# Kernel optimization log

Measured on AMD Instinct MI355X. Metric: run time of the kernel, lower is better.

## Reference

```python
import jax, jax.numpy as jnp
import numpy as np
from jax import lax

B, C, H, W = 16, 128, 64, 64
S = 16  # d_state


def setup_inputs() -> dict:
    key = jax.random.key(0)
    ks = jax.random.split(key, 12)
    d = {
        'x': jax.random.normal(ks[0], (B, C, H, W), jnp.float32),
        'conv_w': jax.random.normal(ks[1], (C, C, 3, 3), jnp.float32) * (1.0 / np.sqrt(C * 9)),
        'conv_b': jax.random.normal(ks[2], (C,), jnp.float32) * 0.01,
        'dt_w': jax.random.normal(ks[3], (C, C), jnp.float32) * (1.0 / np.sqrt(C)),
        'dt_b': jax.random.normal(ks[4], (C,), jnp.float32) * 0.01,
        'A': jax.random.normal(ks[5], (C, S), jnp.float32),
        'D': jax.random.normal(ks[6], (C,), jnp.float32),
        'g1_w': jax.random.normal(ks[7], (C, C), jnp.float32) * (1.0 / np.sqrt(C)),
        'g1_b': jax.random.normal(ks[8], (C,), jnp.float32) * 0.01,
        'g2_w': jax.random.normal(ks[9], (C, C), jnp.float32) * (1.0 / np.sqrt(C)),
        'g2_b': jax.random.normal(ks[10], (C,), jnp.float32) * 0.01,
    }
    return d


def _forward(x, conv_w, conv_b, dt_w, dt_b, A, D, g1_w, g1_b, g2_w, g2_b):
    identity = x
    # 3x3 conv, padding=1 (SAME)
    x = lax.conv_general_dilated(x, conv_w, (1, 1), 'SAME',
                                 dimension_numbers=('NCHW', 'OIHW', 'NCHW'))
    x = x + conv_b[None, :, None, None]
    # spectral gate: global avg pool -> 1x1 conv -> relu -> 1x1 conv -> sigmoid
    pooled = jnp.mean(x, axis=(2, 3))                       # [B, C]
    g = jax.nn.relu(jnp.einsum('bc,oc->bo', pooled, g1_w) + g1_b)
    g = jax.nn.sigmoid(jnp.einsum('bc,oc->bo', g, g2_w) + g2_b)
    x = x * g[:, :, None, None]
    # ssm scan over H*W tokens
    x_seq = x.transpose(0, 2, 3, 1).reshape(x.shape[0], H * W, C)  # [B, L, C]
    dt = jax.nn.sigmoid(jnp.einsum('blc,oc->blo', x_seq, dt_w) + dt_b)
    An = -jnp.exp(A)   # [C, S]
    Dp = jnp.exp(D)    # [C]

    def step(h, inp):
        xt, dtt = inp  # each [B, C]
        h = h * jnp.exp(An[None] * dtt[:, :, None]) + xt[:, :, None]  # [B, C, S]
        y = jnp.sum(h * An[None], axis=-1) + Dp * xt                   # [B, C]
        return h, y

    h0 = jnp.zeros((x.shape[0], C, S), x.dtype)
    xs = (x_seq.transpose(1, 0, 2), dt.transpose(1, 0, 2))  # [L, B, C]
    _, ys = lax.scan(step, h0, xs)                           # ys: [L, B, C]
    y = ys.transpose(1, 0, 2).reshape(x.shape[0], H, W, C).transpose(0, 3, 1, 2)
    return y + identity


def reference(x, conv_w, conv_b, dt_w, dt_b, A, D, g1_w, g1_b, g2_w, g2_b):
    return _forward(x, conv_w, conv_b, dt_w, dt_b, A, D, g1_w, g1_b, g2_w, g2_b)
```

## Files before the change

kernel.cpp:

```cpp
#include <hip/hip_runtime.h>
#include <hip/hip_bf16.h>
#include <stdint.h>

#define BB 16
#define CC 128
#define HH 64
#define WW 64
#define LL 4096
#define SS 16
#define NCH 64
#define CT 64

typedef __attribute__((ext_vector_type(2))) float f32x2;
typedef __attribute__((ext_vector_type(4))) float f32x4;
typedef __attribute__((ext_vector_type(8))) short short8;
typedef __attribute__((ext_vector_type(4))) unsigned int u32x4;

#define AS1 __attribute__((address_space(1)))
#define AS3 __attribute__((address_space(3)))

__device__ __forceinline__ float bf2f(unsigned short u) {
    union { unsigned int i; float f; } v;
    v.i = ((unsigned int)u) << 16;
    return v.f;
}
__device__ __forceinline__ float asf(unsigned int u) {
    union { unsigned int i; float f; } v;
    v.i = u;
    return v.f;
}
__device__ __forceinline__ unsigned short f2bf(float f) {
    union { float f; unsigned int i; } v;
    v.f = f;
    unsigned int x = v.i;
    return (unsigned short)((x + 0x7fffu + ((x >> 16) & 1u)) >> 16);
}
__device__ __forceinline__ float fexp2(float x) { return __builtin_amdgcn_exp2f(x); }

__global__ __launch_bounds__(256) void k0(const float* __restrict__ x, unsigned short* __restrict__ xT,
                                          const float* __restrict__ conv_w, const float* __restrict__ dt_w,
                                          const float* __restrict__ A, const float* __restrict__ Dv,
                                          const float* __restrict__ g1w, const float* __restrict__ g2w,
                                          short* __restrict__ wf, short* __restrict__ wdtf,
                                          float* __restrict__ An, float* __restrict__ An2, float* __restrict__ Dp,
                                          float* __restrict__ pooled, float* __restrict__ g1wT, float* __restrict__ g2wT) {
    __shared__ float lt[64][65];
    int bid = blockIdx.x;
    int tid = threadIdx.x;
    if (bid < 2048) {
        int b = bid >> 7, rem = bid & 127;
        int tt = rem >> 1, ct = rem & 1;
        int t0 = tt * 64, c0 = ct * 64;
        int colr = tid & 63, rowb = tid >> 6;
#pragma unroll
        for (int r = 0; r < 16; ++r) {
            int row = rowb + r * 4;
            lt[row][colr] = x[(size_t)(b * CC + c0 + row) * LL + t0 + colr];
        }
        __syncthreads();
#pragma unroll
        for (int r = 0; r < 16; ++r) {
            int trow = rowb + r * 4;
            xT[((size_t)b * LL + t0 + trow) * CC + c0 + colr] = f2bf(lt[colr][trow]);
        }
        return;
    }
    int idx = (bid - 2048) * 256 + tid;
    if (idx < 18432) {
        int lane = idx & 63, fr = idx >> 6;
        int nfg = fr & 7, ks = (fr >> 3) & 3, tp = fr >> 5;
        int dy = tp / 3, dx = tp % 3;
        int cout = nfg * 16 + (lane & 15);
        int cin0 = ks * 32 + (lane >> 4) * 8;
        short8 v;
#pragma unroll
        for (int j = 0; j < 8; ++j)
            v[j] = (short)f2bf(conv_w[((cout * CC + cin0 + j) * 3 + dy) * 3 + dx]);
        *(short8*)(wf + (size_t)idx * 8) = v;
    } else if (idx < 20480) {
        int i2 = idx - 18432;
        int lane = i2 & 63, fr = i2 >> 6;
        int nfg = fr & 7, ks = fr >> 3;
        int o = nfg * 16 + (lane & 15);
        int c0 = ks * 32 + (lane >> 4) * 8;
        short8 v;
#pragma unroll
        for (int j = 0; j < 8; ++j) v[j] = (short)f2bf(dt_w[o * CC + c0 + j]);
        *(short8*)(wdtf + (size_t)i2 * 8) = v;
    } else if (idx < 22528) {
        int i3 = idx - 20480;
        float a = -expf(A[i3]);
        An[i3] = a;
        An2[i3] = a * 1.4426950408889634f;
    } else if (idx < 22656) {
        int c = idx - 22528;
        Dp[c] = expf(Dv[c]);
    } else if (idx < 24704) {
        pooled[idx - 22656] = 0.f;
    } else if (idx < 41088) {
        int i = idx - 24704;
        int c = i >> 7, o = i & 127;
        g1wT[i] = g1w[o * 128 + c];
    } else if (idx < 57472) {
        int i = idx - 41088;
        int c = i >> 7, o = i & 127;
        g2wT[i] = g2w[o * 128 + c];
    }
}

__global__ __launch_bounds__(256) void k1(const unsigned short* __restrict__ xT,
                                          const short* __restrict__ wf,
                                          const float* __restrict__ conv_b,
                                          unsigned short* __restrict__ convT,
                                          float* __restrict__ pooled) {
    __shared__ __align__(16) unsigned short slab[3 * 66 * 128];
    int bid = blockIdx.x;
    int b = bid >> 6, h = bid & 63;
    int tid = threadIdx.x;
    int wave = tid >> 6, lane = tid & 63;

    if (tid < 96) {
        int dy = tid >> 5, r = (tid >> 4) & 1, j = tid & 15;
        u32x4 z = {0, 0, 0, 0};
        *(u32x4*)((char*)slab + dy * 16896 + (r ? 16640 : 0) + j * 16) = z;
    }
#pragma unroll
    for (int dy = 0; dy < 3; ++dy) {
        int hs = h + dy - 1;
        char* slabdy = (char*)slab + dy * 16896;
        if (hs >= 0 && hs < HH) {
            const char* src = (const char*)xT + (size_t)(b * LL + hs * 64) * 256;
#pragma unroll
            for (int i = 0; i < 4; ++i) {
                unsigned int Xbase = 256u + (unsigned)i * 4096u + (unsigned)wave * 1024u;
                unsigned int X = Xbase + (unsigned)lane * 16u;
                unsigned int tok = X >> 8;
                unsigned int srcoff = ((X & ~255u) - 256u) | ((X & 255u) ^ ((tok & 7u) << 4));
                __builtin_amdgcn_global_load_lds((const AS1 unsigned int*)(src + srcoff),
                                                 (AS3 unsigned int*)(slabdy + Xbase), 16, 0, 0);
            }
        } else {
            u32x4 z = {0, 0, 0, 0};
#pragma unroll
            for (int i = 0; i < 4; ++i)
                *(u32x4*)(slabdy + 256 + tid * 64 + i * 16) = z;
        }
    }
    __syncthreads();

    int lm = lane & 15, lg = lane >> 4;
    f32x4 acc[4][2];
#pragma unroll
    for (int m = 0; m < 4; ++m)
#pragma unroll
        for (int n = 0; n < 2; ++n) acc[m][n] = (f32x4){0.f, 0.f, 0.f, 0.f};

#pragma unroll
    for (int tp = 0; tp < 9; ++tp) {
        int dy = tp / 3, dx = tp % 3;
        const char* slabdy = (const char*)slab + dy * 16896;
#pragma unroll
        for (int ks = 0; ks < 4; ++ks) {
            short8 bf0 = *(const short8*)(wf + ((size_t)(((tp * 4 + ks) * 8) + wave * 2 + 0) * 64 + lane) * 8);
            short8 bf1 = *(const short8*)(wf + ((size_t)(((tp * 4 + ks) * 8) + wave * 2 + 1) * 64 + lane) * 8);
#pragma unroll
            for (int mf = 0; mf < 4; ++mf) {
                int tok = mf * 16 + lm + dx;
                unsigned int off = (unsigned)((tok * 256 + ks * 64 + lg * 16) ^ ((tok & 7) << 4));
                short8 af = *(const short8*)(slabdy + off);
                acc[mf][0] = __builtin_amdgcn_mfma_f32_16x16x32_bf16(af, bf0, acc[mf][0], 0, 0, 0);
                acc[mf][1] = __builtin_amdgcn_mfma_f32_16x16x32_bf16(af, bf1, acc[mf][1], 0, 0, 0);
            }
        }
    }

    int n0w = wave * 32;
    size_t tokbase = (size_t)(b * LL + h * 64);
    float psum[2] = {0.f, 0.f};
#pragma unroll
    for (int nf = 0; nf < 2; ++nf) {
        int n = n0w + nf * 16 + lm;
        float bias = conv_b[n];
#pragma unroll
        for (int mf = 0; mf < 4; ++mf)
#pragma unroll
            for (int r = 0; r < 4; ++r) {
                int w = mf * 16 + lg * 4 + r;
                float v = acc[mf][nf][r] + bias;
                convT[(tokbase + w) * CC + n] = f2bf(v);
                psum[nf] += v;
            }
    }
#pragma unroll
    for (int nf = 0; nf < 2; ++nf) {
        float s = psum[nf];
        s += __shfl_xor(s, 16);
        s += __shfl_xor(s, 32);
        if (lane < 16) atomicAdd(&pooled[b * CC + n0w + nf * 16 + lane], s);
    }
}

__global__ __launch_bounds__(256) void k3(const unsigned short* __restrict__ convT,
                                          const short* __restrict__ wdtf,
                                          const float* __restrict__ pooled,
                                          const float* __restrict__ g1wT, const float* __restrict__ g1b,
                                          const float* __restrict__ g2wT, const float* __restrict__ g2b,
                                          float* __restrict__ gate,
                                          const float* __restrict__ dt_b,
                                          const float* __restrict__ An2,
                                          unsigned short* __restrict__ dtT,
                                          unsigned int* __restrict__ xdt,
                                          float* __restrict__ hend, float* __restrict__ decay,
                                          int packed) {
    __shared__ __align__(16) unsigned short albuf[128 * 128];
    __shared__ __align__(16) unsigned short dtl[128 * 136];
    __shared__ float gl[128];
    float* meanr = (float*)dtl;
    float* garr  = ((float*)dtl) + 128;
    int bid = blockIdx.x;
    int b = bid >> 5, tile = bid & 31, t0 = tile * 128;
    int tid = threadIdx.x;
    int wave = tid >> 6, lane = tid & 63;

    if (tid < 128) meanr[tid] = pooled[b * CC + tid] * (1.f / 4096.f);
    __syncthreads();
    if (tid < 128) {
        float acc = g1b[tid];
        for (int c = 0; c < 128; ++c) acc += meanr[c] * g1wT[c * 128 + tid];
        garr[tid] = fmaxf(acc, 0.f);
    }
    __syncthreads();
    if (tid < 128) {
        float acc2 = g2b[tid];
        for (int c = 0; c < 128; ++c) acc2 += garr[c] * g2wT[c * 128 + tid];
        float gv = __builtin_amdgcn_rcpf(1.f + fexp2(-1.4426950408889634f * acc2));
        gl[tid] = gv;
        if (tile == 0) gate[b * CC + tid] = gv;
    }
    __syncthreads();

    const char* srcb = (const char*)convT + (size_t)(b * LL + t0) * 256;
#pragma unroll
    for (int i = 0; i < 8; ++i) {
        unsigned int byteoff = (unsigned)((i * 256 + tid) * 16);
        unsigned int tok = byteoff >> 8;
        unsigned int inner = byteoff & 255u;
        int c8 = (int)(inner >> 1);
        short8 v = *(const short8*)(srcb + (size_t)tok * 256 + inner);
#pragma unroll
        for (int j = 0; j < 8; ++j) {
            float f = bf2f((unsigned short)v[j]) * gl[c8 + j];
            v[j] = (short)f2bf(f);
        }
        *(short8*)((char*)albuf + (byteoff ^ ((tok & 7u) << 4))) = v;
    }
    __syncthreads();

    int lm = lane & 15, lg = lane >> 4;
    f32x4 acc[8][2];
#pragma unroll
    for (int m = 0; m < 8; ++m)
#pragma unroll
        for (int n = 0; n < 2; ++n) acc[m][n] = (f32x4){0.f, 0.f, 0.f, 0.f};
#pragma unroll
    for (int ks = 0; ks < 4; ++ks) {
        short8 bf0 = *(const short8*)(wdtf + ((size_t)((ks * 8) + wave * 2 + 0) * 64 + lane) * 8);
        short8 bf1 = *(const short8*)(wdtf + ((size_t)((ks * 8) + wave * 2 + 1) * 64 + lane) * 8);
#pragma unroll
        for (int mf = 0; mf < 8; ++mf) {
            int tok = mf * 16 + lm;
            unsigned int off = (unsigned)((tok * 256 + ks * 64 + lg * 16) ^ ((tok & 7) << 4));
            short8 af = *(const short8*)((const char*)albuf + off);
            acc[mf][0] = __builtin_amdgcn_mfma_f32_16x16x32_bf16(af, bf0, acc[mf][0], 0, 0, 0);
            acc[mf][1] = __builtin_amdgcn_mfma_f32_16x16x32_bf16(af, bf1, acc[mf][1], 0, 0, 0);
        }
    }
    __syncthreads();
#pragma unroll
    for (int nf = 0; nf < 2; ++nf) {
        int o = wave * 32 + nf * 16 + lm;
        float zb = dt_b[o];
#pragma unroll
        for (int mf = 0; mf < 8; ++mf)
#pragma unroll
            for (int r = 0; r < 4; ++r) {
                int tok = mf * 16 + lg * 4 + r;
                float z = acc[mf][nf][r] + zb;
                float d = __builtin_amdgcn_rcpf(1.f + fexp2(-1.4426950408889634f * z));
                unsigned short ub = f2bf(d);
                if (!packed) dtT[(size_t)(b * LL + t0 + tok) * CC + o] = ub;
                dtl[tok * 136 + o] = ub;
            }
    }
    __syncthreads();

    if (packed) {
        unsigned int* xdblk = xdt + ((size_t)b * LL + t0) * CC;
        int tq = tid >> 5, c0 = (tid & 31) * 4;
#pragma unroll
        for (int k = 0; k < 16; ++k) {
            int t = k * 8 + tq;
            unsigned int xoff = ((unsigned)(t * 256 + c0 * 2)) ^ (((unsigned)t & 7u) << 4);
            const unsigned short* xu4 = (const unsigned short*)((const char*)albuf + xoff);
            const unsigned short* du4 = &dtl[t * 136 + c0];
            u32x4 w4;
#pragma unroll
            for (int j = 0; j < 4; ++j)
                w4[j] = (((unsigned int)du4[j]) << 16) | (unsigned int)xu4[j];
            *(u32x4*)(xdblk + (size_t)t * CC + c0) = w4;
        }
    }

    int half = tid >> 7, c = tid & 127;
    int ch = tile * 2 + half;
    float a2[SS], h[SS];
#pragma unroll
    for (int s = 0; s < SS; ++s) {
        a2[s] = An2[c * SS + s];
        h[s] = 0.f;
    }
    float sdt = 0.f;
#pragma unroll 4
    for (int t = 0; t < CT; ++t) {
        int tokb = half * 64 + t;
        unsigned int xoff = ((unsigned)(tokb * 256 + c * 2)) ^ (((unsigned)tokb & 7u) << 4);
        float x = bf2f(*(const unsigned short*)((const char*)albuf + xoff));
        float d = bf2f(dtl[tokb * 136 + c]);
        sdt += d;
#pragma unroll
        for (int s = 0; s < SS; ++s) h[s] = h[s] * fexp2(a2[s] * d) + x;
    }
    size_t base = ((size_t)(b * NCH + ch) * CC + c) * SS;
#pragma unroll
    for (int q = 0; q < 4; ++q) {
        f32x4 hv, dv;
#pragma unroll
        for (int j = 0; j < 4; ++j) {
            hv[j] = h[q * 4 + j];
            dv[j] = fexp2(a2[q * 4 + j] * sdt);
        }
        *(f32x4*)(hend + base + q * 4) = hv;
        *(f32x4*)(decay + base + q * 4) = dv;
    }
}

__global__ __launch_bounds__(256) void k5(const float* __restrict__ hend, const float* __restrict__ decay,
                                          float* __restrict__ H0) {
    int idx = blockIdx.x * 256 + threadIdx.x;
    int b = idx >> 11, rem = idx & 2047;
    float Hv = 0.f;
    for (int k = 0; k < NCH; ++k) {
        size_t base = (size_t)(b * NCH + k) * 2048 + rem;
        H0[base] = Hv;
        Hv = hend[base] + Hv * decay[base];
    }
}

__global__ __launch_bounds__(256, 4) void k6p(const unsigned int* __restrict__ xdt,
                                              const float* __restrict__ Antab,
                                              const float* __restrict__ An2tab,
                                              const float* __restrict__ Dp,
                                              const float* __restrict__ H0,
                                              const float* __restrict__ xin,
                                              float* __restrict__ out) {
    __shared__ unsigned short ylds[128][66];
    int bid = blockIdx.x;
    int b = bid >> 6, ch = bid & 63;
    int tid = threadIdx.x;
    int wave = tid >> 6, lane = tid & 63;
    int t0 = ch * CT;
    int c = wave * 32 + (lane & 31);
    int shalf = lane >> 5;
    int s0 = shalf * 8;

    f32x2 a22[4], anv[4], h2[4];
#pragma unroll
    for (int q = 0; q < 2; ++q) {
        f32x4 av = *(const f32x4*)(An2tab + c * SS + s0 + q * 4);
        f32x4 nv = *(const f32x4*)(Antab + c * SS + s0 + q * 4);
        a22[q * 2 + 0] = (f32x2){av[0], av[1]};
        a22[q * 2 + 1] = (f32x2){av[2], av[3]};
        anv[q * 2 + 0] = (f32x2){nv[0], nv[1]};
        anv[q * 2 + 1] = (f32x2){nv[2], nv[3]};
    }
    size_t hbase = ((size_t)(b * NCH + ch) * CC + c) * SS + s0;
#pragma unroll
    for (int q = 0; q < 2; ++q) {
        f32x4 hv = *(const f32x4*)(H0 + hbase + q * 4);
        h2[q * 2 + 0] = (f32x2){hv[0], hv[1]};
        h2[q * 2 + 1] = (f32x2){hv[2], hv[3]};
    }
    float dpc = (shalf == 0) ? Dp[c] : 0.f;
    const unsigned int* xdp = xdt + ((size_t)b * LL + t0) * CC + c;

#pragma unroll 8
    for (int t = 0; t < CT; ++t) {
        unsigned int w = xdp[(size_t)t * CC];
        float x = asf(w << 16);
        float d = asf(w & 0xffff0000u);
        f32x2 x2 = {x, x};
        f32x2 d2 = {d, d};
        f32x2 y2 = {0.f, 0.f};
#pragma unroll
        for (int q = 0; q < 4; ++q) {
            f32x2 tq = a22[q] * d2;
            f32x2 e2;
            e2.x = fexp2(tq.x);
            e2.y = fexp2(tq.y);
            h2[q] = h2[q] * e2 + x2;
            y2 += h2[q] * anv[q];
        }
        float yp = y2.x + y2.y + dpc * x;
        float yo = yp + __shfl_xor(yp, 32);
        if (shalf == 0) ylds[c][t] = f2bf(yo);
    }
    __syncthreads();

    int tt = tid & 63, wq = tid >> 6;
    size_t outbase = (size_t)b * CC * LL + t0 + tt;
#pragma unroll 4
    for (int rr = 0; rr < 32; ++rr) {
        int row = rr * 4 + wq;
        size_t gi = outbase + (size_t)row * LL;
        out[gi] = bf2f(ylds[row][tt]) + xin[gi];
    }
}

__global__ __launch_bounds__(256, 4) void k6f(const unsigned short* __restrict__ convT,
                                              const unsigned short* __restrict__ dtT,
                                              const float* __restrict__ gate,
                                              const float* __restrict__ Antab,
                                              const float* __restrict__ An2tab,
                                              const float* __restrict__ Dp,
                                              const float* __restrict__ H0,
                                              const float* __restrict__ xin,
                                              float* __restrict__ out) {
    __shared__ unsigned short ylds[128][66];
    int bid = blockIdx.x;
    int b = bid >> 6, ch = bid & 63;
    int tid = threadIdx.x;
    int wave = tid >> 6, lane = tid & 63;
    int t0 = ch * CT;
    int c = wave * 32 + (lane & 31);
    int shalf = lane >> 5;
    int s0 = shalf * 8;

    float a2[8], an[8], h[8];
#pragma unroll
    for (int q = 0; q < 2; ++q) {
        f32x4 av = *(const f32x4*)(An2tab + c * SS + s0 + q * 4);
        f32x4 nv = *(const f32x4*)(Antab + c * SS + s0 + q * 4);
#pragma unroll
        for (int j = 0; j < 4; ++j) { a2[q * 4 + j] = av[j]; an[q * 4 + j] = nv[j]; }
    }
    size_t hbase = ((size_t)(b * NCH + ch) * CC + c) * SS + s0;
#pragma unroll
    for (int q = 0; q < 2; ++q) {
        f32x4 hv = *(const f32x4*)(H0 + hbase + q * 4);
#pragma unroll
        for (int j = 0; j < 4; ++j) h[q * 4 + j] = hv[j];
    }
    float g = gate[b * CC + c];
    float dpc = (shalf == 0) ? Dp[c] : 0.f;
    const unsigned short* xp = convT + (size_t)(b * LL + t0) * CC + c;
    const unsigned short* dp = dtT + (size_t)(b * LL + t0) * CC + c;

#pragma unroll 4
    for (int t = 0; t < CT; ++t) {
        float x = bf2f(xp[t * CC]) * g;
        float d = bf2f(dp[t * CC]);
        float y0 = dpc * x, y1 = 0.f;
#pragma unroll
        for (int s = 0; s < 8; ++s) {
            h[s] = h[s] * fexp2(a2[s] * d) + x;
            if (s & 1) y1 += h[s] * an[s]; else y0 += h[s] * an[s];
        }
        float yp = y0 + y1;
        float yo = yp + __shfl_xor(yp, 32);
        if (shalf == 0) ylds[c][t] = f2bf(yo);
    }
    __syncthreads();

    int tt = tid & 63, wq = tid >> 6;
    size_t outbase = (size_t)b * CC * LL + t0 + tt;
#pragma unroll 4
    for (int rr = 0; rr < 32; ++rr) {
        int row = rr * 4 + wq;
        size_t gi = outbase + (size_t)row * LL;
        out[gi] = bf2f(ylds[row][tt]) + xin[gi];
    }
}

extern "C" void kernel_launch(void* const* d_in, const int* in_sizes, int n_in,
                              void* d_out, int out_size, void* d_ws, size_t ws_size,
                              hipStream_t stream) {
    const float* x      = (const float*)d_in[0];
    const float* conv_w = (const float*)d_in[1];
    const float* conv_b = (const float*)d_in[2];
    const float* dt_w   = (const float*)d_in[3];
    const float* dt_b   = (const float*)d_in[4];
    const float* A      = (const float*)d_in[5];
    const float* D      = (const float*)d_in[6];
    const float* g1w    = (const float*)d_in[7];
    const float* g1b    = (const float*)d_in[8];
    const float* g2w    = (const float*)d_in[9];
    const float* g2b    = (const float*)d_in[10];
    float* outp         = (float*)d_out;
    char* ws = (char*)d_ws;

    const bool P = (ws_size >= 67600896ull);

    unsigned short* xT;
    float *hend, *decay, *H0, *g1wT, *g2wT, *pooled, *gate, *Antab, *An2tab, *Dp;
    unsigned short *convT, *dtT;
    unsigned int* xdt;
    short *wf, *wdtf;

    if (P) {
        xT     = (unsigned short*)(ws + 0);
        hend   = (float*)(ws + 0);
        decay  = (float*)(ws + 8388608);
        convT  = (unsigned short*)(ws + 16777216);
        H0     = (float*)(ws + 16777216);
        xdt    = (unsigned int*)(ws + 33554432);
        dtT    = (unsigned short*)(ws + 33554432);
        wf     = (short*)(ws + 67108864);
        wdtf   = (short*)(ws + 67403776);
        pooled = (float*)(ws + 67436544);
        gate   = (float*)(ws + 67444736);
        Antab  = (float*)(ws + 67452928);
        An2tab = (float*)(ws + 67461120);
        Dp     = (float*)(ws + 67469312);
        g1wT   = (float*)(ws + 67469824);
        g2wT   = (float*)(ws + 67535360);
    } else {
        xT     = (unsigned short*)(ws + 0);
        hend   = (float*)(ws + 0);
        decay  = (float*)(ws + 8388608);
        convT  = (unsigned short*)(ws + 16777216);
        dtT    = (unsigned short*)(ws + 33554432);
        xdt    = (unsigned int*)(ws + 33554432);
        H0     = (float*)(ws + 50331648);
        g1wT   = (float*)(ws + 50331648);
        g2wT   = (float*)(ws + 50397184);
        wf     = (short*)(ws + 58720256);
        wdtf   = (short*)(ws + 59015168);
        pooled = (float*)(ws + 59047936);
        gate   = (float*)(ws + 59056128);
        Antab  = (float*)(ws + 59064320);
        An2tab = (float*)(ws + 59072512);
        Dp     = (float*)(ws + 59080704);
    }

    hipLaunchKernelGGL(k0, dim3(2273), dim3(256), 0, stream, x, xT, conv_w, dt_w, A, D, g1w, g2w,
                       wf, wdtf, Antab, An2tab, Dp, pooled, g1wT, g2wT);
    hipLaunchKernelGGL(k1, dim3(1024), dim3(256), 0, stream, xT, wf, conv_b, convT, pooled);
    hipLaunchKernelGGL(k3, dim3(512), dim3(256), 0, stream, convT, wdtf, pooled, g1wT, g1b, g2wT, g2b,
                       gate, dt_b, An2tab, dtT, xdt, hend, decay, (int)P);
    hipLaunchKernelGGL(k5, dim3(128), dim3(256), 0, stream, hend, decay, H0);
    if (P) {
        hipLaunchKernelGGL(k6p, dim3(1024), dim3(256), 0, stream, (const unsigned int*)xdt,
                           Antab, An2tab, Dp, H0, x, outp);
    } else {
        hipLaunchKernelGGL(k6f, dim3(1024), dim3(256), 0, stream, convT, dtT, gate,
                           Antab, An2tab, Dp, H0, x, outp);
    }
}
```

Measured before the change: 127.1 us.

## Split gate MLP into own kernel and halve k3 tile with state-dim split

Moves the spectral-gate MLP out of k3 into a small k2 kernel (16 blocks), so k3 no longer recomputes the gate MLP redundantly in every block. k3 now processes 64-token chunks across 1024 blocks instead of 128-token tiles across 512 blocks. The per-chunk scan splits the 16 state dims between the two thread halves rather than splitting tokens. This cuts redundant work and shared memory per block and raises parallelism, at the cost of an extra kernel launch and a serial dependency on k2.

```diff
diff --git a/kernel.cpp b/kernel.cpp
--- a/kernel.cpp
+++ b/kernel.cpp
@@ -200,48 +200,48 @@
     }
 }
 
+__global__ __launch_bounds__(128) void k2(const float* __restrict__ pooled,
+                                          const float* __restrict__ g1wT, const float* __restrict__ g1b,
+                                          const float* __restrict__ g2wT, const float* __restrict__ g2b,
+                                          float* __restrict__ gate) {
+    __shared__ float meanr[128];
+    __shared__ float garr[128];
+    int b = blockIdx.x;
+    int tid = threadIdx.x;
+    meanr[tid] = pooled[b * CC + tid] * (1.f / 4096.f);
+    __syncthreads();
+    float acc = g1b[tid];
+    for (int c = 0; c < 128; ++c) acc += meanr[c] * g1wT[c * 128 + tid];
+    garr[tid] = fmaxf(acc, 0.f);
+    __syncthreads();
+    float acc2 = g2b[tid];
+    for (int c = 0; c < 128; ++c) acc2 += garr[c] * g2wT[c * 128 + tid];
+    gate[b * CC + tid] = __builtin_amdgcn_rcpf(1.f + fexp2(-1.4426950408889634f * acc2));
+}
+
 __global__ __launch_bounds__(256) void k3(const unsigned short* __restrict__ convT,
                                           const short* __restrict__ wdtf,
-                                          const float* __restrict__ pooled,
-                                          const float* __restrict__ g1wT, const float* __restrict__ g1b,
-                                          const float* __restrict__ g2wT, const float* __restrict__ g2b,
-                                          float* __restrict__ gate,
+                                          const float* __restrict__ gate,
                                           const float* __restrict__ dt_b,
                                           const float* __restrict__ An2,
                                           unsigned short* __restrict__ dtT,
                                           unsigned int* __restrict__ xdt,
                                           float* __restrict__ hend, float* __restrict__ decay,
                                           int packed) {
-    __shared__ __align__(16) unsigned short albuf[128 * 128];
-    __shared__ __align__(16) unsigned short dtl[128 * 136];
+    __shared__ __align__(16) unsigned short albuf[64 * 128];
+    __shared__ __align__(16) unsigned short dtl[64 * 136];
     __shared__ float gl[128];
-    float* meanr = (float*)dtl;
-    float* garr  = ((float*)dtl) + 128;
     int bid = blockIdx.x;
-    int b = bid >> 5, tile = bid & 31, t0 = tile * 128;
+    int b = bid >> 6, ch = bid & 63, t0 = ch * 64;
     int tid = threadIdx.x;
     int wave = tid >> 6, lane = tid & 63;
 
-    if (tid < 128) meanr[tid] = pooled[b * CC + tid] * (1.f / 4096.f);
-    __syncthreads();
-    if (tid < 128) {
-        float acc = g1b[tid];
-        for (int c = 0; c < 128; ++c) acc += meanr[c] * g1wT[c * 128 + tid];
-        garr[tid] = fmaxf(acc, 0.f);
-    }
-    __syncthreads();
-    if (tid < 128) {
-        float acc2 = g2b[tid];
-        for (int c = 0; c < 128; ++c) acc2 += garr[c] * g2wT[c * 128 + tid];
-        float gv = __builtin_amdgcn_rcpf(1.f + fexp2(-1.4426950408889634f * acc2));
-        gl[tid] = gv;
-        if (tile == 0) gate[b * CC + tid] = gv;
-    }
+    if (tid < 128) gl[tid] = gate[b * CC + tid];
     __syncthreads();
 
     const char* srcb = (const char*)convT + (size_t)(b * LL + t0) * 256;
 #pragma unroll
-    for (int i = 0; i < 8; ++i) {
+    for (int i = 0; i < 4; ++i) {
         unsigned int byteoff = (unsigned)((i * 256 + tid) * 16);
         unsigned int tok = byteoff >> 8;
         unsigned int inner = byteoff & 255u;
@@ -257,9 +257,9 @@
     __syncthreads();
 
     int lm = lane & 15, lg = lane >> 4;
-    f32x4 acc[8][2];
-#pragma unroll
-    for (int m = 0; m < 8; ++m)
+    f32x4 acc[4][2];
+#pragma unroll
+    for (int m = 0; m < 4; ++m)
 #pragma unroll
         for (int n = 0; n < 2; ++n) acc[m][n] = (f32x4){0.f, 0.f, 0.f, 0.f};
 #pragma unroll
@@ -267,7 +267,7 @@
         short8 bf0 = *(const short8*)(wdtf + ((size_t)((ks * 8) + wave * 2 + 0) * 64 + lane) * 8);
         short8 bf1 = *(const short8*)(wdtf + ((size_t)((ks * 8) + wave * 2 + 1) * 64 + lane) * 8);
 #pragma unroll
-        for (int mf = 0; mf < 8; ++mf) {
+        for (int mf = 0; mf < 4; ++mf) {
             int tok = mf * 16 + lm;
             unsigned int off = (unsigned)((tok * 256 + ks * 64 + lg * 16) ^ ((tok & 7) << 4));
             short8 af = *(const short8*)((const char*)albuf + off);
@@ -275,13 +275,12 @@
             acc[mf][1] = __builtin_amdgcn_mfma_f32_16x16x32_bf16(af, bf1, acc[mf][1], 0, 0, 0);
         }
     }
-    __syncthreads();
 #pragma unroll
     for (int nf = 0; nf < 2; ++nf) {
         int o = wave * 32 + nf * 16 + lm;
         float zb = dt_b[o];
 #pragma unroll
-        for (int mf = 0; mf < 8; ++mf)
+        for (int mf = 0; mf < 4; ++mf)
 #pragma unroll
             for (int r = 0; r < 4; ++r) {
                 int tok = mf * 16 + lg * 4 + r;
@@ -298,7 +297,7 @@
         unsigned int* xdblk = xdt + ((size_t)b * LL + t0) * CC;
         int tq = tid >> 5, c0 = (tid & 31) * 4;
 #pragma unroll
-        for (int k = 0; k < 16; ++k) {
+        for (int k = 0; k < 8; ++k) {
             int t = k * 8 + tq;
             unsigned int xoff = ((unsigned)(t * 256 + c0 * 2)) ^ (((unsigned)t & 7u) << 4);
             const unsigned short* xu4 = (const unsigned short*)((const char*)albuf + xoff);
@@ -311,28 +310,27 @@
         }
     }
 
-    int half = tid >> 7, c = tid & 127;
-    int ch = tile * 2 + half;
-    float a2[SS], h[SS];
-#pragma unroll
-    for (int s = 0; s < SS; ++s) {
-        a2[s] = An2[c * SS + s];
-        h[s] = 0.f;
+    int c = tid & 127, shalf = tid >> 7, s0 = shalf * 8;
+    float a2[8], h[8];
+#pragma unroll
+    for (int q = 0; q < 2; ++q) {
+        f32x4 av = *(const f32x4*)(An2 + c * SS + s0 + q * 4);
+#pragma unroll
+        for (int j = 0; j < 4; ++j) { a2[q * 4 + j] = av[j]; h[q * 4 + j] = 0.f; }
     }
     float sdt = 0.f;
 #pragma unroll 4
     for (int t = 0; t < CT; ++t) {
-        int tokb = half * 64 + t;
-        unsigned int xoff = ((unsigned)(tokb * 256 + c * 2)) ^ (((unsigned)tokb & 7u) << 4);
+        unsigned int xoff = ((unsigned)(t * 256 + c * 2)) ^ (((unsigned)t & 7u) << 4);
         float x = bf2f(*(const unsigned short*)((const char*)albuf + xoff));
-        float d = bf2f(dtl[tokb * 136 + c]);
+        float d = bf2f(dtl[t * 136 + c]);
         sdt += d;
 #pragma unroll
-        for (int s = 0; s < SS; ++s) h[s] = h[s] * fexp2(a2[s] * d) + x;
-    }
-    size_t base = ((size_t)(b * NCH + ch) * CC + c) * SS;
-#pragma unroll
-    for (int q = 0; q < 4; ++q) {
+        for (int s = 0; s < 8; ++s) h[s] = h[s] * fexp2(a2[s] * d) + x;
+    }
+    size_t base = ((size_t)(b * NCH + ch) * CC + c) * SS + s0;
+#pragma unroll
+    for (int q = 0; q < 2; ++q) {
         f32x4 hv, dv;
 #pragma unroll
         for (int j = 0; j < 4; ++j) {
@@ -555,8 +553,9 @@
     hipLaunchKernelGGL(k0, dim3(2273), dim3(256), 0, stream, x, xT, conv_w, dt_w, A, D, g1w, g2w,
                        wf, wdtf, Antab, An2tab, Dp, pooled, g1wT, g2wT);
     hipLaunchKernelGGL(k1, dim3(1024), dim3(256), 0, stream, xT, wf, conv_b, convT, pooled);
-    hipLaunchKernelGGL(k3, dim3(512), dim3(256), 0, stream, convT, wdtf, pooled, g1wT, g1b, g2wT, g2b,
-                       gate, dt_b, An2tab, dtT, xdt, hend, decay, (int)P);
+    hipLaunchKernelGGL(k2, dim3(16), dim3(128), 0, stream, pooled, g1wT, g1b, g2wT, g2b, gate);
+    hipLaunchKernelGGL(k3, dim3(1024), dim3(256), 0, stream, convT, wdtf, gate, dt_b, An2tab,
+                       dtT, xdt, hend, decay, (int)P);
     hipLaunchKernelGGL(k5, dim3(128), dim3(256), 0, stream, hend, decay, H0);
     if (P) {
         hipLaunchKernelGGL(k6p, dim3(1024), dim3(256), 0, stream, (const unsigned int*)xdt,
```

New measurement: 126.3 us. About the same (-0.6%).
